# Kernel tuning notes

Hardware: AMD Instinct MI355X
Metric: run time of the kernel (lower is better)

The kernel has to match this reference:

```python
import jax, jax.numpy as jnp
import numpy as np

N, M, A, F = 8000, 12, 64, 64
EPS = 1e-5


def setup_inputs() -> dict:
    key = jax.random.key(0)
    ks = jax.random.split(key, 8)
    rn = lambda k, s, sc=0.05: jax.random.normal(k, s, jnp.float32) * sc
    return {
        "atom_in_fea": rn(ks[0], (N, A), 1.0),
        "nbr_fea": rn(ks[1], (N, M, F), 1.0),
        "nbr_fea_idx": jax.random.randint(ks[2], (N, M), 0, N),
        # fc_full: in = 2A+F, out = 2A (stored as (in, out))
        "W_full": rn(ks[3], (2 * A + F, 2 * A)), "b_full": jnp.zeros((2 * A,), jnp.float32),
        "bn1_gamma": jnp.ones((2 * A,), jnp.float32), "bn1_beta": jnp.zeros((2 * A,), jnp.float32),
        # fc_edge: in = 2A+F, out = 2F
        "W_edge": rn(ks[4], (2 * A + F, 2 * F)), "b_edge": jnp.zeros((2 * F,), jnp.float32),
        "bne_gamma": jnp.ones((2 * F,), jnp.float32), "bne_beta": jnp.zeros((2 * F,), jnp.float32),
        # fc_3body: in = 3A+2F, out = 2A
        "W_3body": rn(ks[5], (3 * A + 2 * F, 2 * A)), "b_3body": jnp.zeros((2 * A,), jnp.float32),
        "bn3_gamma": jnp.ones((2 * A,), jnp.float32), "bn3_beta": jnp.zeros((2 * A,), jnp.float32),
        # bn2 over atom_fea_len
        "bn2_gamma": jnp.ones((A,), jnp.float32), "bn2_beta": jnp.zeros((A,), jnp.float32),
    }


def _bn(x, gamma, beta):
    # training-mode BatchNorm1d: batch stats over all but the last (channel) axis, biased var
    axes = tuple(range(x.ndim - 1))
    mean = jnp.mean(x, axes, keepdims=True)
    var = jnp.mean(jnp.square(x - mean), axes, keepdims=True)
    return (x - mean) * jax.lax.rsqrt(var + EPS) * gamma + beta


def _gate(z, axis):
    filt, core = jnp.split(z, 2, axis=-1)
    return jnp.sum(jax.nn.sigmoid(filt) * jax.nn.softplus(core), axis=axis)


def reference(atom_in_fea, nbr_fea, nbr_fea_idx,
              W_full, b_full, bn1_gamma, bn1_beta,
              W_edge, b_edge, bne_gamma, bne_beta,
              W_3body, b_3body, bn3_gamma, bn3_beta,
              bn2_gamma, bn2_beta):
    a_len = atom_in_fea.shape[1]
    f_len = nbr_fea.shape[2]
    atom_nbr = atom_in_fea[nbr_fea_idx]                       # (N, M, A) gather
    total = jnp.concatenate([
        jnp.broadcast_to(atom_in_fea[:, None, :], atom_nbr.shape),
        atom_nbr, nbr_fea], axis=-1)                           # (N, M, 2A+F)

    # 2-body gated update
    g = _bn(total @ W_full + b_full, bn1_gamma, bn1_beta)      # (N, M, 2A)
    two_body = _gate(g, axis=1)                                # (N, A)

    # explicit edge update
    e = _bn(total @ W_edge + b_edge, bne_gamma, bne_beta)      # (N, M, 2F)
    ef, ec = jnp.split(e, 2, axis=-1)
    nbr_out_fea = nbr_fea + jax.nn.sigmoid(ef) * jax.nn.softplus(ec)

    # 3-body term: Linear over concat([x_i, x_j, x_l, e_ij, e_il]) decomposed so we never
    # materialize the (N, M, M, 3A+2F) concat; only the (N, M, M, 2A) projection exists.
    Wa, Wj, Wl, Wij, Wil = jnp.split(
        W_3body, [a_len, 2 * a_len, 3 * a_len, 3 * a_len + f_len], axis=0)
    p_i = atom_in_fea @ Wa                                     # (N, 2A)
    p_j = atom_nbr @ Wj + nbr_fea @ Wij                        # (N, M, 2A) j/ij part
    p_l = atom_nbr @ Wl + nbr_fea @ Wil                        # (N, M, 2A) l/il part
    z = p_i[:, None, None, :] + p_j[:, :, None, :] + p_l[:, None, :, :] + b_3body
    z = _bn(z, bn3_gamma, bn3_beta)                            # (N, M, M, 2A)
    three_body = _gate(z, axis=(1, 2))                         # (N, A)

    total_summed = _bn(two_body + three_body, bn2_gamma, bn2_beta)
    atom_out_fea = jax.nn.softplus(atom_in_fea + total_summed)
    return (atom_out_fea, nbr_out_fea)
```

## Files before the change

kernel.cpp:

```cpp
#include <hip/hip_runtime.h>

typedef unsigned short u16;
typedef unsigned int u32;
typedef __attribute__((ext_vector_type(8))) short short8;
typedef __attribute__((ext_vector_type(4))) float f32x4;

#define NATOMS 8000
#define MNBR 12
#define EPSV 1e-5f
#define AB 4
#define ROWS 48
#define NBLK 2000
#define K2REC 1664

#define STG_B 12672
__device__ __forceinline__ int stg_idx(int row, int col) {
  return (row >> 2) * 528 + (row & 3) * 128 + col;
}

#define XB_OFF 0
#define WTA_OFF 1024000
#define WTE_OFF 1122304
#define WAT_OFF 1187840
#define SSUM_OFF 1220608
#define PARAMS_OFF 1227776
#define TBUF_OFF 1230848
#define WS_NEED 3278848

#define SS_BN1S 0
#define SS_BN1S2 128
#define SS_BNES 256
#define SS_BNES2 384
#define SS_U2 512
#define SS_V2 640
#define SS_A 768
#define SS_A2 896
#define SS_UB 1024
#define SS_VB 1152
#define SS_AU 1280
#define SS_AV 1408
#define SS_UV 1536

__device__ __forceinline__ u16 f2bf(float f) {
  u32 u = __float_as_uint(f);
  u += 0x7FFFu + ((u >> 16) & 1u);
  return (u16)(u >> 16);
}
__device__ __forceinline__ float bf2f(u16 h) { return __uint_as_float(((u32)h) << 16); }

__device__ __forceinline__ float sigf(float x) {
  return __builtin_amdgcn_rcpf(1.f + __expf(-x));
}
__device__ __forceinline__ float spf(float x) {
  return fmaxf(x, 0.f) + __logf(1.f + __expf(-fabsf(x)));
}

__device__ __forceinline__ void mfma16(f32x4 &acc, short8 a, short8 b) {
  asm volatile("v_mfma_f32_16x16x32_bf16 %0, %1, %2, %0" : "+v"(acc) : "v"(a), "v"(b));
}
__device__ __forceinline__ void accfence(f32x4 &a) {
  asm volatile("s_nop 7\ns_nop 7\ns_nop 7" : "+v"(a));
}
__device__ __forceinline__ void initfence(f32x4 &a) {
  asm volatile("s_nop 1" : "+v"(a));
}

__device__ __forceinline__ void stage_row16(short* lds, int row, int c16, const float* __restrict__ src) {
  const float4* s4 = reinterpret_cast<const float4*>(src);
  float4 q0 = s4[0], q1 = s4[1], q2 = s4[2], q3 = s4[3];
  short8 lo, hi;
  lo[0]=(short)f2bf(q0.x); lo[1]=(short)f2bf(q0.y); lo[2]=(short)f2bf(q0.z); lo[3]=(short)f2bf(q0.w);
  lo[4]=(short)f2bf(q1.x); lo[5]=(short)f2bf(q1.y); lo[6]=(short)f2bf(q1.z); lo[7]=(short)f2bf(q1.w);
  hi[0]=(short)f2bf(q2.x); hi[1]=(short)f2bf(q2.y); hi[2]=(short)f2bf(q2.z); hi[3]=(short)f2bf(q2.w);
  hi[4]=(short)f2bf(q3.x); hi[5]=(short)f2bf(q3.y); hi[6]=(short)f2bf(q3.z); hi[7]=(short)f2bf(q3.w);
  int base = row * 128 + c16 * 2;
  int sw = (row & 7) << 4;
  *reinterpret_cast<short8*>(reinterpret_cast<char*>(lds) + (base ^ sw)) = lo;
  *reinterpret_cast<short8*>(reinterpret_cast<char*>(lds) + ((base + 16) ^ sw)) = hi;
}

__device__ __forceinline__ void stage_xj(const u16* __restrict__ XB, const int* __restrict__ nidx,
                                         int eb, int ab, char* xjT, int t) {
  for (int s = t; s < 512; s += 256) {
    int r = s >> 3, j = s & 7;
    uint4 val = make_uint4(0u, 0u, 0u, 0u);
    if (r < 48) {
      int idx = nidx[eb + r];
      val = *reinterpret_cast<const uint4*>(XB + (size_t)idx * 64 + j * 8);
    } else if (r < 52) {
      val = *reinterpret_cast<const uint4*>(XB + (size_t)(ab + r - 48) * 64 + j * 8);
    }
    int off = (r * 128 + j * 16) ^ ((r & 7) << 4);
    *reinterpret_cast<uint4*>(xjT + off) = val;
  }
}

__device__ __forceinline__ short8 lds_afrag(const char* lds, int row, int kbyte) {
  int off = (row * 128 + kbyte) ^ ((row & 7) << 4);
  return *reinterpret_cast<const short8*>(lds + off);
}

template <int RT>
__device__ __forceinline__ void mfma_dual(const char* xjT, const char* nbrT,
                                          const u16* __restrict__ WTA, const u16* __restrict__ WTE,
                                          int baseA, int baseE, int w, int l,
                                          f32x4 (&acc)[RT][2]) {
  short8 ba[2][2], be[2][2];
#pragma unroll
  for (int p = 0; p < 2; ++p) {
    int colg = ((w + p * 4) << 4) + (l & 15);
#pragma unroll
    for (int kc = 0; kc < 2; ++kc) {
      ba[p][kc] = *reinterpret_cast<const short8*>(WTA + (size_t)(baseA + colg) * 64 + kc * 32 + ((l >> 4) << 3));
      be[p][kc] = *reinterpret_cast<const short8*>(WTE + (size_t)(baseE + colg) * 64 + kc * 32 + ((l >> 4) << 3));
    }
  }
#pragma unroll
  for (int rt = 0; rt < RT; ++rt)
#pragma unroll
    for (int p = 0; p < 2; ++p) { acc[rt][p] = f32x4{0.f, 0.f, 0.f, 0.f}; initfence(acc[rt][p]); }
#pragma unroll
  for (int rt = 0; rt < RT; ++rt) {
    int arow = rt * 16 + (l & 15);
    short8 x0 = lds_afrag(xjT, arow, (l >> 4) << 4);
    short8 x1 = lds_afrag(xjT, arow, 64 + ((l >> 4) << 4));
    short8 n0 = lds_afrag(nbrT, arow, (l >> 4) << 4);
    short8 n1 = lds_afrag(nbrT, arow, 64 + ((l >> 4) << 4));
#pragma unroll
    for (int p = 0; p < 2; ++p) {
      mfma16(acc[rt][p], x0, ba[p][0]);
      mfma16(acc[rt][p], x1, ba[p][1]);
      mfma16(acc[rt][p], n0, be[p][0]);
      mfma16(acc[rt][p], n1, be[p][1]);
    }
  }
#pragma unroll
  for (int rt = 0; rt < RT; ++rt)
#pragma unroll
    for (int p = 0; p < 2; ++p) accfence(acc[rt][p]);
}

__device__ __forceinline__ void mfma_own(const char* xjT, const u16* __restrict__ WTA,
                                         int baseO, int w, int l, float* ownv) {
  short8 bo[2][2];
#pragma unroll
  for (int p = 0; p < 2; ++p) {
    int colg = ((w + p * 4) << 4) + (l & 15);
#pragma unroll
    for (int kc = 0; kc < 2; ++kc)
      bo[p][kc] = *reinterpret_cast<const short8*>(WTA + (size_t)(baseO + colg) * 64 + kc * 32 + ((l >> 4) << 3));
  }
  int arow = 48 + (l & 15);
  short8 x0 = lds_afrag(xjT, arow, (l >> 4) << 4);
  short8 x1 = lds_afrag(xjT, arow, 64 + ((l >> 4) << 4));
  f32x4 acc[2];
#pragma unroll
  for (int p = 0; p < 2; ++p) {
    acc[p] = f32x4{0.f, 0.f, 0.f, 0.f};
    initfence(acc[p]);
    mfma16(acc[p], x0, bo[p][0]);
    mfma16(acc[p], x1, bo[p][1]);
  }
#pragma unroll
  for (int p = 0; p < 2; ++p) accfence(acc[p]);
  if (l < 16) {
    int col0 = (w << 4) + l;
#pragma unroll
    for (int r = 0; r < 4; ++r) {
      ownv[r * 128 + col0] = acc[0][r];
      ownv[r * 128 + col0 + 64] = acc[1][r];
    }
  }
}

__device__ __forceinline__ void aterm_dot(const float* __restrict__ WaT, const float* xown,
                                          int c, int h, float& dv0, float& dv1) {
  const float4* wa4 = reinterpret_cast<const float4*>(WaT + (size_t)c * 64);
  const float4* x0 = reinterpret_cast<const float4*>(xown + (2 * h) * 64);
  const float4* x1 = reinterpret_cast<const float4*>(xown + (2 * h + 1) * 64);
  dv0 = 0.f; dv1 = 0.f;
#pragma unroll
  for (int q = 0; q < 16; ++q) {
    float4 wv = wa4[q], a4 = x0[q], b4 = x1[q];
    dv0 += a4.x * wv.x + a4.y * wv.y + a4.z * wv.z + a4.w * wv.w;
    dv1 += b4.x * wv.x + b4.y * wv.y + b4.z * wv.z + b4.w * wv.w;
  }
}

__global__ __launch_bounds__(256) void k0_prep(const float* __restrict__ atom_in,
                                               const float* __restrict__ W_full,
                                               const float* __restrict__ W_edge,
                                               const float* __restrict__ W_3body,
                                               u16* __restrict__ XB,
                                               u16* __restrict__ WTA, u16* __restrict__ WTE,
                                               float* __restrict__ WaT,
                                               float* __restrict__ ssum) {
  int t = blockIdx.x * 256 + threadIdx.x;
  if (t < 1792) ssum[t] = 0.f;
  if (t < 8192) { int c = t >> 6, k = t & 63; WaT[t] = W_3body[k * 128 + c]; }
  if (t < 49152) {
    int col = t >> 6, k = t & 63;
    int blk = col >> 7, c = col & 127;
    float v;
    switch (blk) {
      case 0: v = W_full[k * 128 + c]; break;
      case 1: v = W_full[(64 + k) * 128 + c]; break;
      case 2: v = W_edge[k * 128 + c]; break;
      case 3: v = W_edge[(64 + k) * 128 + c]; break;
      case 4: v = W_3body[(64 + k) * 128 + c]; break;
      default: v = W_3body[(128 + k) * 128 + c]; break;
    }
    WTA[t] = f2bf(v);
  } else if (t < 81920) {
    int u = t - 49152;
    int col = u >> 6, k = u & 63;
    int blk = col >> 7, c = col & 127;
    float v;
    switch (blk) {
      case 0: v = W_full[(128 + k) * 128 + c]; break;
      case 1: v = W_edge[(128 + k) * 128 + c]; break;
      case 2: v = W_3body[(192 + k) * 128 + c]; break;
      default: v = W_3body[(256 + k) * 128 + c]; break;
    }
    WTE[u] = f2bf(v);
  }
  if (t < NATOMS * 64) XB[t] = f2bf(atom_in[t]);
}

__global__ __launch_bounds__(256, 4) void k2_stats(const float* __restrict__ atom_in,
                                                   const float* __restrict__ nbr_fea,
                                                   const int* __restrict__ nidx,
                                                   const float* __restrict__ WaT,
                                                   const float* __restrict__ b_full,
                                                   const float* __restrict__ b_edge,
                                                   const float* __restrict__ b_3body,
                                                   const u16* __restrict__ XB,
                                                   const u16* __restrict__ WTA,
                                                   const u16* __restrict__ WTE,
                                                   float* __restrict__ k2scr) {
  __shared__ __align__(16) char smem[25088];
  char* nbrT    = smem;
  char* xjT     = smem + 6144;
  float* ownv   = (float*)(smem + 14336);
  float* ubar   = (float*)(smem + 16384);
  float* vbar   = (float*)(smem + 18432);
  float* xown   = (float*)(smem + 20480);
  float* redscr = (float*)(smem + 21504);
  int t = threadIdx.x, l = t & 63, w = t >> 6;
  int ab = blockIdx.x * AB, eb = ab * 12;
  float* sc = k2scr + (size_t)blockIdx.x * K2REC;

  for (int u = t; u < ROWS * 4; u += 256) {
    int row = u >> 2, c16 = (u & 3) * 16;
    stage_row16((short*)nbrT, row, c16, nbr_fea + (size_t)(eb + row) * 64 + c16);
  }
  stage_xj(XB, nidx, eb, ab, xjT, t);
  ubar[t] = 0.f; ubar[256 + t] = 0.f; vbar[t] = 0.f; vbar[256 + t] = 0.f;
  xown[t] = atom_in[(size_t)ab * 64 + t];
  __syncthreads();

  const int baseA[4] = {128, 384, 512, 640};
#pragma unroll
  for (int b = 0; b < 4; ++b) {
    f32x4 acc[3][2];
    mfma_dual<3>(xjT, nbrT, WTA, WTE, baseA[b], b * 128, w, l, acc);
    int col0 = (w << 4) + (l & 15), col1 = col0 + 64;
    int g = l >> 4;
    if (b < 2) {
      mfma_own(xjT, WTA, b ? 256 : 0, w, l, ownv);
      const float* bp = b ? b_edge : b_full;
      float bias0 = bp[col0], bias1 = bp[col1];
      float vs0 = 0.f, vs1 = 0.f, q0 = 0.f, q1 = 0.f;
#pragma unroll
      for (int rt = 0; rt < 3; ++rt) {
        int a12 = (rt * 16 + g * 4) / 12;
        float o0 = ownv[a12 * 128 + col0] + bias0;
        float o1 = ownv[a12 * 128 + col1] + bias1;
#pragma unroll
        for (int r = 0; r < 4; ++r) {
          float v0 = acc[rt][0][r] + o0;
          float v1 = acc[rt][1][r] + o1;
          vs0 += v0; q0 += v0 * v0; vs1 += v1; q1 += v1 * v1;
        }
      }
      vs0 += __shfl_xor(vs0, 16); vs0 += __shfl_xor(vs0, 32);
      vs1 += __shfl_xor(vs1, 16); vs1 += __shfl_xor(vs1, 32);
      q0 += __shfl_xor(q0, 16); q0 += __shfl_xor(q0, 32);
      q1 += __shfl_xor(q1, 16); q1 += __shfl_xor(q1, 32);
      if (l < 16) {
        int base = b ? 256 : 0;
        sc[base + col0] = vs0;
        sc[base + 128 + col0] = q0;
        sc[base + col1] = vs1;
        sc[base + 128 + col1] = q1;
      }
    } else {
      float* uvb = (b == 2) ? ubar : vbar;
      float q0 = 0.f, q1 = 0.f;
#pragma unroll
      for (int rt = 0; rt < 3; ++rt) {
        int a12 = (rt * 16 + g * 4) / 12;
        float s0 = 0.f, s1 = 0.f;
#pragma unroll
        for (int r = 0; r < 4; ++r) {
          float v0 = acc[rt][0][r];
          float v1 = acc[rt][1][r];
          s0 += v0; q0 += v0 * v0; s1 += v1; q1 += v1 * v1;
        }
        atomicAdd(&uvb[a12 * 128 + col0], s0);
        atomicAdd(&uvb[a12 * 128 + col1], s1);
      }
      q0 += __shfl_xor(q0, 16); q0 += __shfl_xor(q0, 32);
      q1 += __shfl_xor(q1, 16); q1 += __shfl_xor(q1, 32);
      if (l < 16) {
        int base = (b == 2) ? SS_U2 : SS_V2;
        sc[base + col0] = q0;
        sc[base + col1] = q1;
      }
    }
  }
  __syncthreads();

  {
    int c = t & 127, h = t >> 7;
    float dv0, dv1;
    aterm_dot(WaT, xown, c, h, dv0, dv1);
    float b3v = b_3body[c];
    float pA = 0.f, pA2 = 0.f, pUb = 0.f, pVb = 0.f, pAU = 0.f, pAV = 0.f, pUV = 0.f;
#pragma unroll
    for (int aa = 0; aa < 2; ++aa) {
      int a = 2 * h + aa;
      float aval = (aa ? dv1 : dv0) + b3v;
      float ub = ubar[a * 128 + c] * (1.f / 12.f);
      float vb = vbar[a * 128 + c] * (1.f / 12.f);
      pA += aval; pA2 += aval * aval; pUb += ub; pVb += vb;
      pAU += aval * ub; pAV += aval * vb; pUV += ub * vb;
    }
    if (h == 1) {
      float* rs = &redscr[c * 7];
      rs[0] = pA; rs[1] = pA2; rs[2] = pUb; rs[3] = pVb; rs[4] = pAU; rs[5] = pAV; rs[6] = pUV;
    }
    __syncthreads();
    if (h == 0) {
      const float* rs = &redscr[c * 7];
      sc[SS_A + c] = pA + rs[0];
      sc[SS_A2 + c] = pA2 + rs[1];
      sc[SS_UB + c] = pUb + rs[2];
      sc[SS_VB + c] = pVb + rs[3];
      sc[SS_AU + c] = pAU + rs[4];
      sc[SS_AV + c] = pAV + rs[5];
      sc[SS_UV + c] = pUV + rs[6];
    }
  }
}

__global__ __launch_bounds__(256) void k3r_reduce(const float* __restrict__ k2scr,
                                                  float* __restrict__ ssum) {
  int cb = blockIdx.x & 1, ch = blockIdx.x >> 1;
  int f = cb * 256 + threadIdx.x;
  if (f >= K2REC / 4) return;
  int r0 = ch * 32;
  if (r0 >= NBLK) return;
  int r1 = min(r0 + 32, NBLK);
  float s0 = 0.f, s1 = 0.f, s2 = 0.f, s3 = 0.f;
#pragma unroll 8
  for (int r = r0; r < r1; ++r) {
    float4 v = *reinterpret_cast<const float4*>(k2scr + (size_t)r * K2REC + f * 4);
    s0 += v.x; s1 += v.y; s2 += v.z; s3 += v.w;
  }
  atomicAdd(&ssum[f * 4 + 0], s0);
  atomicAdd(&ssum[f * 4 + 1], s1);
  atomicAdd(&ssum[f * 4 + 2], s2);
  atomicAdd(&ssum[f * 4 + 3], s3);
}

__global__ void k3p_params(const float* __restrict__ ssum,
                           const float* __restrict__ g1, const float* __restrict__ be1,
                           const float* __restrict__ ge, const float* __restrict__ bee,
                           const float* __restrict__ g3, const float* __restrict__ be3,
                           float* __restrict__ params) {
  int c = threadIdx.x;
  if (c >= 128) return;
  const float cnt1 = 1.f / 96000.f;
  {
    float m = ssum[SS_BN1S + c] * cnt1;
    float var = ssum[SS_BN1S2 + c] * cnt1 - m * m;
    float s = g1[c] * rsqrtf(fmaxf(var, 0.f) + EPSV);
    params[c] = s; params[128 + c] = be1[c] - m * s;
  }
  {
    float m = ssum[SS_BNES + c] * cnt1;
    float var = ssum[SS_BNES2 + c] * cnt1 - m * m;
    float s = ge[c] * rsqrtf(fmaxf(var, 0.f) + EPSV);
    params[256 + c] = s; params[384 + c] = bee[c] - m * s;
  }
  {
    float Nf = (float)NATOMS;
    float A_ = ssum[SS_A + c], A2 = ssum[SS_A2 + c];
    float U2 = ssum[SS_U2 + c], V2 = ssum[SS_V2 + c];
    float Ub = ssum[SS_UB + c], Vb = ssum[SS_VB + c];
    float AU = ssum[SS_AU + c], AV = ssum[SS_AV + c], UV = ssum[SS_UV + c];
    float m = (A_ + Ub + Vb) / Nf;
    float ez2 = A2 / Nf + (U2 + V2) / (Nf * 12.f) + 2.f * (AU + AV + UV) / Nf;
    float var = ez2 - m * m;
    float s = g3[c] * rsqrtf(fmaxf(var, 0.f) + EPSV);
    params[512 + c] = s; params[640 + c] = be3[c] - m * s;
  }
}

__global__ __launch_bounds__(256, 4) void k4_main(const float* __restrict__ atom_in,
                                                  const float* __restrict__ nbr_fea,
                                                  const int* __restrict__ nidx,
                                                  const float* __restrict__ WaT,
                                                  const float* __restrict__ b_full,
                                                  const float* __restrict__ b_edge,
                                                  const float* __restrict__ b_3body,
                                                  const u16* __restrict__ XB,
                                                  const u16* __restrict__ WTA,
                                                  const u16* __restrict__ WTE,
                                                  const float* __restrict__ params,
                                                  float* __restrict__ tbuf,
                                                  float* __restrict__ out_nbr,
                                                  float* __restrict__ bn2scr) {
  __shared__ __align__(16) char smem[36224];
  char* nbrT      = smem;
  char* xjT       = smem + 6144;
  u16* u_s        = (u16*)(smem + 14336);
  float* ownv     = (float*)(smem + 27008);
  float* t2buf    = (float*)(smem + 29056);
  float* params_s = (float*)(smem + 30080);
  float* p3_s     = (float*)(smem + 32128);
  float* a_s      = (float*)(smem + 33152);
  float* xown     = (float*)(smem + 35200);
  u16* v_s        = (u16*)smem;
  float* redscr2  = (float*)(smem + 14336);
  int t = threadIdx.x, l = t & 63, w = t >> 6;
  int ab = blockIdx.x * AB, eb = ab * 12;

  for (int u = t; u < ROWS * 4; u += 256) {
    int row = u >> 2, c16 = (u & 3) * 16;
    stage_row16((short*)nbrT, row, c16, nbr_fea + (size_t)(eb + row) * 64 + c16);
  }
  stage_xj(XB, nidx, eb, ab, xjT, t);
  xown[t] = atom_in[(size_t)ab * 64 + t];
  params_s[t] = params[t];
  params_s[t + 256] = params[t + 256];
  p3_s[t] = params[512 + t];
  t2buf[t] = 0.f;
  __syncthreads();

  {
    int c = t & 127, h = t >> 7;
    float dv0, dv1;
    aterm_dot(WaT, xown, c, h, dv0, dv1);
    float s3 = p3_s[c], t3 = p3_s[128 + c];
    float b3v = b_3body[c];
    a_s[(2 * h) * 128 + c] = (dv0 + b3v) * s3 + t3;
    a_s[(2 * h + 1) * 128 + c] = (dv1 + b3v) * s3 + t3;
  }

#pragma unroll
  for (int b = 0; b < 2; ++b) {
    f32x4 acc[3][2];
    mfma_dual<3>(xjT, nbrT, WTA, WTE, b ? 384 : 128, b * 128, w, l, acc);
    mfma_own(xjT, WTA, b ? 256 : 0, w, l, ownv);
    int col0 = (w << 4) + (l & 15), col1 = col0 + 64;
    int g = l >> 4;
    const float* bp = b ? b_edge : b_full;
    float bias0 = bp[col0], bias1 = bp[col1];
    float sc0 = params_s[b * 256 + col0], sh0 = params_s[b * 256 + 128 + col0];
    float sc1 = params_s[b * 256 + col1], sh1 = params_s[b * 256 + 128 + col1];
#pragma unroll
    for (int rt = 0; rt < 3; ++rt) {
      int a12 = (rt * 16 + g * 4) / 12;
      float o0 = ownv[a12 * 128 + col0] + bias0;
      float o1 = ownv[a12 * 128 + col1] + bias1;
      float gsum = 0.f;
#pragma unroll
      for (int r = 0; r < 4; ++r) {
        int row = rt * 16 + g * 4 + r;
        float v0 = acc[rt][0][r] + o0;
        float v1 = acc[rt][1][r] + o1;
        float gate = sigf(v0 * sc0 + sh0) * spf(v1 * sc1 + sh1);
        if (b == 0) {
          gsum += gate;
        } else {
          size_t eg = (size_t)(eb + row) * 64 + col0;
          out_nbr[eg] = nbr_fea[eg] + gate;
        }
      }
      if (b == 0) atomicAdd(&t2buf[a12 * 64 + col0], gsum);
    }
  }

  {
    f32x4 acc[3][2];
    mfma_dual<3>(xjT, nbrT, WTA, WTE, 512, 256, w, l, acc);
    int col0 = (w << 4) + (l & 15), col1 = col0 + 64;
    int g = l >> 4;
    float s30 = p3_s[col0], s31 = p3_s[col1];
#pragma unroll
    for (int rt = 0; rt < 3; ++rt) {
#pragma unroll
      for (int r = 0; r < 4; ++r) {
        int row = rt * 16 + g * 4 + r;
        u_s[stg_idx(row, col0)] = f2bf(acc[rt][0][r] * s30);
        u_s[stg_idx(row, col1)] = f2bf(acc[rt][1][r] * s31);
      }
    }
  }
  {
    f32x4 acc[3][2];
    mfma_dual<3>(xjT, nbrT, WTA, WTE, 640, 384, w, l, acc);
    __syncthreads();
    int col0 = (w << 4) + (l & 15), col1 = col0 + 64;
    int g = l >> 4;
    float s30 = p3_s[col0], s31 = p3_s[col1];
#pragma unroll
    for (int rt = 0; rt < 3; ++rt) {
#pragma unroll
      for (int r = 0; r < 4; ++r) {
        int row = rt * 16 + g * 4 + r;
        v_s[stg_idx(row, col0)] = f2bf(acc[rt][0][r] * s30);
        v_s[stg_idx(row, col1)] = f2bf(acc[rt][1][r] * s31);
      }
    }
  }
  __syncthreads();

  float acc3 = 0.f;
  {
    int c = l, a = w;
    float af = a_s[a * 128 + c], ac = a_s[a * 128 + 64 + c];
    float Fl[12], Hl[12];
#pragma unroll
    for (int j2 = 0; j2 < 12; ++j2) {
      float vf = bf2f(v_s[stg_idx(a * 12 + j2, c)]);
      float vc = bf2f(v_s[stg_idx(a * 12 + j2, 64 + c)]);
      Fl[j2] = __expf(-vf);
      Hl[j2] = __expf(vc);
    }
    for (int j = 0; j < 12; ++j) {
      float uf = bf2f(u_s[stg_idx(a * 12 + j, c)]);
      float uc = bf2f(u_s[stg_idx(a * 12 + j, 64 + c)]);
      float Ej = __expf(-(af + uf));
      float Gj = __expf(ac + uc);
#pragma unroll
      for (int l2 = 0; l2 < 12; ++l2) {
        float p = fmaf(Ej, Fl[l2], 1.f);
        float q = fmaf(Gj, Hl[l2], 1.f);
        acc3 += __builtin_amdgcn_rcpf(p) * __log2f(q);
      }
    }
  }
  __syncthreads();

  {
    float x = t2buf[t] + acc3 * 0.6931471805599453f;
    tbuf[(size_t)(ab + w) * 64 + l] = x;
    redscr2[t] = x;
    redscr2[256 + t] = x * x;
    __syncthreads();
    if (t < 64) {
      float s = redscr2[t] + redscr2[t + 64] + redscr2[t + 128] + redscr2[t + 192];
      float s2 = redscr2[256 + t] + redscr2[256 + t + 64] + redscr2[256 + t + 128] + redscr2[256 + t + 192];
      bn2scr[(size_t)t * 2048 + blockIdx.x] = s;
      bn2scr[(size_t)(64 + t) * 2048 + blockIdx.x] = s2;
    }
  }
}

__global__ __launch_bounds__(256) void k5_reduce(const float* __restrict__ bn2scr,
                                                 float* __restrict__ bn2sum) {
  __shared__ float wsum[4];
  int c = blockIdx.x, t = threadIdx.x;
  float s = 0.f;
#pragma unroll 4
  for (int i = t; i < NBLK; i += 256) s += bn2scr[(size_t)c * 2048 + i];
  s += __shfl_xor(s, 1); s += __shfl_xor(s, 2); s += __shfl_xor(s, 4);
  s += __shfl_xor(s, 8); s += __shfl_xor(s, 16); s += __shfl_xor(s, 32);
  if ((t & 63) == 0) wsum[t >> 6] = s;
  __syncthreads();
  if (t == 0) bn2sum[c] = wsum[0] + wsum[1] + wsum[2] + wsum[3];
}

__global__ __launch_bounds__(256) void k6_out(const float* __restrict__ atom_in,
                                              const float* __restrict__ tbuf,
                                              const float* __restrict__ bn2sum,
                                              const float* __restrict__ g2,
                                              const float* __restrict__ be2,
                                              float* __restrict__ out_atom) {
  __shared__ float sc[64], sh[64];
  int t = threadIdx.x;
  if (t < 64) {
    float S = bn2sum[t], S2 = bn2sum[64 + t];
    float m = S * (1.f / (float)NATOMS);
    float var = S2 * (1.f / (float)NATOMS) - m * m;
    float s = g2[t] * rsqrtf(fmaxf(var, 0.f) + EPSV);
    sc[t] = s; sh[t] = be2[t] - m * s;
  }
  __syncthreads();
  int i = blockIdx.x * 256 + t;
  if (i < NATOMS * 64) {
    int c = i & 63;
    float v = atom_in[i] + tbuf[i] * sc[c] + sh[c];
    out_atom[i] = spf(v);
  }
}

extern "C" void kernel_launch(void* const* d_in, const int* in_sizes, int n_in,
                              void* d_out, int out_size, void* d_ws, size_t ws_size,
                              hipStream_t stream) {
  if (ws_size < (size_t)WS_NEED) return;
  const float* atom_in = (const float*)d_in[0];
  const float* nbr_fea = (const float*)d_in[1];
  const int* nidx = (const int*)d_in[2];
  const float* W_full = (const float*)d_in[3];
  const float* b_full = (const float*)d_in[4];
  const float* g1 = (const float*)d_in[5];
  const float* be1 = (const float*)d_in[6];
  const float* W_edge = (const float*)d_in[7];
  const float* b_edge = (const float*)d_in[8];
  const float* ge = (const float*)d_in[9];
  const float* bee = (const float*)d_in[10];
  const float* W_3body = (const float*)d_in[11];
  const float* b_3body = (const float*)d_in[12];
  const float* g3 = (const float*)d_in[13];
  const float* be3 = (const float*)d_in[14];
  const float* g2 = (const float*)d_in[15];
  const float* be2 = (const float*)d_in[16];

  char* ws = (char*)d_ws;
  u16* XB = (u16*)(ws + XB_OFF);
  u16* WTA = (u16*)(ws + WTA_OFF);
  u16* WTE = (u16*)(ws + WTE_OFF);
  float* WaT = (float*)(ws + WAT_OFF);
  float* ssum = (float*)(ws + SSUM_OFF);
  float* bn2sum = ssum + K2REC;
  float* params = (float*)(ws + PARAMS_OFF);
  float* tbuf = (float*)(ws + TBUF_OFF);

  float* out_atom = (float*)d_out;
  float* out_nbr = out_atom + NATOMS * 64;
  float* k2scr = out_nbr;
  float* bn2scr = out_atom;

  k0_prep<<<2000, 256, 0, stream>>>(atom_in, W_full, W_edge, W_3body, XB, WTA, WTE, WaT, ssum);
  k2_stats<<<NBLK, 256, 0, stream>>>(atom_in, nbr_fea, nidx, WaT, b_full, b_edge, b_3body,
                                     XB, WTA, WTE, k2scr);
  k3r_reduce<<<128, 256, 0, stream>>>(k2scr, ssum);
  k3p_params<<<1, 128, 0, stream>>>(ssum, g1, be1, ge, bee, g3, be3, params);
  k4_main<<<NBLK, 256, 0, stream>>>(atom_in, nbr_fea, nidx, WaT, b_full, b_edge, b_3body,
                                    XB, WTA, WTE, params, tbuf, out_nbr, bn2scr);
  k5_reduce<<<128, 256, 0, stream>>>(bn2scr, bn2sum);
  k6_out<<<2000, 256, 0, stream>>>(atom_in, tbuf, bn2sum, g2, be2, out_atom);
}
```

Measured before the change: 169.2 us.

## Compute BN statistics via Gram matrix of edge inputs instead of per-edge projections

Replaces the stats pass, which projected every edge through all weight blocks, with one that accumulates a 128x128 Gram matrix of concatenated [x_j, e_ij] inputs plus per-atom sums. Second moments then come from w^T M w in a small new kernel, and first moments and cross terms from projecting per-atom sums. This cuts the stats-pass MFMA work and register pressure, at the cost of global atomics into 8 replicated Gram copies, two extra small kernels, and bf16 rounding of summed inputs. The quadratic-form step also changes numerical behaviour compared with direct accumulation.

Measured after the change: 164.3 us. 1.03x faster.

```diff
diff --git a/kernel.cpp b/kernel.cpp
--- a/kernel.cpp
+++ b/kernel.cpp
@@ -11,7 +11,8 @@
 #define AB 4
 #define ROWS 48
 #define NBLK 2000
-#define K2REC 1664
+#define NZG 500
+#define KREC 1408
 
 #define STG_B 12672
 __device__ __forceinline__ int stg_idx(int row, int col) {
@@ -20,26 +21,27 @@
 
 #define XB_OFF 0
 #define WTA_OFF 1024000
-#define WTE_OFF 1122304
-#define WAT_OFF 1187840
-#define SSUM_OFF 1220608
-#define PARAMS_OFF 1227776
-#define TBUF_OFF 1230848
-#define WS_NEED 3278848
+#define WTE_OFF 1138688
+#define WAT_OFF 1204224
+#define MREP_OFF 1236992
+#define MFIN_OFF 1761280
+#define QF4_OFF 1826816
+#define SSUM_OFF 1828864
+#define PARAMS_OFF 1835008
+#define TBUF_OFF 1838080
+#define WS_NEED 3886080
 
 #define SS_BN1S 0
 #define SS_BN1S2 128
 #define SS_BNES 256
 #define SS_BNES2 384
-#define SS_U2 512
-#define SS_V2 640
-#define SS_A 768
-#define SS_A2 896
-#define SS_UB 1024
-#define SS_VB 1152
-#define SS_AU 1280
-#define SS_AV 1408
-#define SS_UV 1536
+#define SS_A 512
+#define SS_A2 640
+#define SS_UB 768
+#define SS_VB 896
+#define SS_AU 1024
+#define SS_AV 1152
+#define SS_UV 1280
 
 __device__ __forceinline__ u16 f2bf(float f) {
   u32 u = __float_as_uint(f);
@@ -100,6 +102,15 @@
   return *reinterpret_cast<const short8*>(lds + off);
 }
 
+__device__ __forceinline__ void zt_w16(char* zT, int chan, int e, u16 v) {
+  int off = (chan * 128 + e * 2) ^ ((chan & 7) << 4);
+  *reinterpret_cast<u16*>(zT + off) = v;
+}
+__device__ __forceinline__ u16 zt_r16(const char* zT, int chan, int e) {
+  int off = (chan * 128 + e * 2) ^ ((chan & 7) << 4);
+  return *reinterpret_cast<const u16*>(zT + off);
+}
+
 template <int RT>
 __device__ __forceinline__ void mfma_dual(const char* xjT, const char* nbrT,
                                           const u16* __restrict__ WTA, const u16* __restrict__ WTE,
@@ -132,6 +143,38 @@
       mfma16(acc[rt][p], x1, ba[p][1]);
       mfma16(acc[rt][p], n0, be[p][0]);
       mfma16(acc[rt][p], n1, be[p][1]);
+    }
+  }
+#pragma unroll
+  for (int rt = 0; rt < RT; ++rt)
+#pragma unroll
+    for (int p = 0; p < 2; ++p) accfence(acc[rt][p]);
+}
+
+template <int RT>
+__device__ __forceinline__ void mfma_single(const char* aT, const u16* __restrict__ WTA,
+                                            int baseC, int w, int l, f32x4 (&acc)[RT][2]) {
+  short8 bw[2][2];
+#pragma unroll
+  for (int p = 0; p < 2; ++p) {
+    int colg = ((w + p * 4) << 4) + (l & 15);
+#pragma unroll
+    for (int kc = 0; kc < 2; ++kc)
+      bw[p][kc] = *reinterpret_cast<const short8*>(WTA + (size_t)(baseC + colg) * 64 + kc * 32 + ((l >> 4) << 3));
+  }
+#pragma unroll
+  for (int rt = 0; rt < RT; ++rt)
+#pragma unroll
+    for (int p = 0; p < 2; ++p) { acc[rt][p] = f32x4{0.f, 0.f, 0.f, 0.f}; initfence(acc[rt][p]); }
+#pragma unroll
+  for (int rt = 0; rt < RT; ++rt) {
+    int arow = rt * 16 + (l & 15);
+    short8 x0 = lds_afrag(aT, arow, (l >> 4) << 4);
+    short8 x1 = lds_afrag(aT, arow, 64 + ((l >> 4) << 4));
+#pragma unroll
+    for (int p = 0; p < 2; ++p) {
+      mfma16(acc[rt][p], x0, bw[p][0]);
+      mfma16(acc[rt][p], x1, bw[p][1]);
     }
   }
 #pragma unroll
@@ -194,11 +237,13 @@
                                                u16* __restrict__ XB,
                                                u16* __restrict__ WTA, u16* __restrict__ WTE,
                                                float* __restrict__ WaT,
+                                               float* __restrict__ Mrep,
                                                float* __restrict__ ssum) {
   int t = blockIdx.x * 256 + threadIdx.x;
-  if (t < 1792) ssum[t] = 0.f;
+  if (t < 1536) ssum[t] = 0.f;
+  if (t < 131072) Mrep[t] = 0.f;
   if (t < 8192) { int c = t >> 6, k = t & 63; WaT[t] = W_3body[k * 128 + c]; }
-  if (t < 49152) {
+  if (t < 57344) {
     int col = t >> 6, k = t & 63;
     int blk = col >> 7, c = col & 127;
     float v;
@@ -208,11 +253,12 @@
       case 2: v = W_edge[k * 128 + c]; break;
       case 3: v = W_edge[(64 + k) * 128 + c]; break;
       case 4: v = W_3body[(64 + k) * 128 + c]; break;
-      default: v = W_3body[(128 + k) * 128 + c]; break;
+      case 5: v = W_3body[(128 + k) * 128 + c]; break;
+      default: v = W_3body[k * 128 + c]; break;
     }
     WTA[t] = f2bf(v);
-  } else if (t < 81920) {
-    int u = t - 49152;
+  } else if (t < 57344 + 32768) {
+    int u = t - 57344;
     int col = u >> 6, k = u & 63;
     int blk = col >> 7, c = col & 127;
     float v;
@@ -227,154 +273,236 @@
   if (t < NATOMS * 64) XB[t] = f2bf(atom_in[t]);
 }
 
-__global__ __launch_bounds__(256, 4) void k2_stats(const float* __restrict__ atom_in,
-                                                   const float* __restrict__ nbr_fea,
-                                                   const int* __restrict__ nidx,
-                                                   const float* __restrict__ WaT,
-                                                   const float* __restrict__ b_full,
-                                                   const float* __restrict__ b_edge,
-                                                   const float* __restrict__ b_3body,
-                                                   const u16* __restrict__ XB,
-                                                   const u16* __restrict__ WTA,
-                                                   const u16* __restrict__ WTE,
-                                                   float* __restrict__ k2scr) {
-  __shared__ __align__(16) char smem[25088];
-  char* nbrT    = smem;
-  char* xjT     = smem + 6144;
-  float* ownv   = (float*)(smem + 14336);
-  float* ubar   = (float*)(smem + 16384);
-  float* vbar   = (float*)(smem + 18432);
-  float* xown   = (float*)(smem + 20480);
-  float* redscr = (float*)(smem + 21504);
+__global__ __launch_bounds__(256, 4) void kzg_stats(const float* __restrict__ nbr_fea,
+                                                    const int* __restrict__ nidx,
+                                                    const float* __restrict__ b_full,
+                                                    const float* __restrict__ b_edge,
+                                                    const float* __restrict__ b_3body,
+                                                    const u16* __restrict__ XB,
+                                                    const u16* __restrict__ WTA,
+                                                    const u16* __restrict__ WTE,
+                                                    float* __restrict__ Mrep,
+                                                    float* __restrict__ krec) {
+  __shared__ __align__(16) char smem[30720];
+  char* zT       = smem;
+  char* xT       = smem + 16384;
+  char* ZxT      = smem + 18432;
+  char* ZnT      = smem + 20480;
+  float* Zbar    = (float*)(smem + 22528);
   int t = threadIdx.x, l = t & 63, w = t >> 6;
-  int ab = blockIdx.x * AB, eb = ab * 12;
-  float* sc = k2scr + (size_t)blockIdx.x * K2REC;
-
-  for (int u = t; u < ROWS * 4; u += 256) {
-    int row = u >> 2, c16 = (u & 3) * 16;
-    stage_row16((short*)nbrT, row, c16, nbr_fea + (size_t)(eb + row) * 64 + c16);
-  }
-  stage_xj(XB, nidx, eb, ab, xjT, t);
-  ubar[t] = 0.f; ubar[256 + t] = 0.f; vbar[t] = 0.f; vbar[256 + t] = 0.f;
-  xown[t] = atom_in[(size_t)ab * 64 + t];
+  int bid = blockIdx.x;
+  int ab = bid * 16;
+  float* sc = krec + (size_t)bid * KREC;
+
+  if (t < 128) {
+    int row = t >> 3, j = t & 7;
+    uint4 val = *reinterpret_cast<const uint4*>(XB + (size_t)(ab + row) * 64 + j * 8);
+    int off = (row * 128 + j * 16) ^ ((row & 7) << 4);
+    *reinterpret_cast<uint4*>(xT + off) = val;
+  }
+  for (int s = t; s < 2048; s += 256) Zbar[s] = 0.f;
+  for (int s = t; s < 512; s += 256) {
+    int chan = s >> 2, kq = 48 + (s & 3) * 4;
+    int off = (chan * 128 + kq * 2) ^ ((chan & 7) << 4);
+    *reinterpret_cast<uint2*>(zT + off) = make_uint2(0u, 0u);
+  }
+
+  f32x4 gacc[2][8];
+#pragma unroll
+  for (int h = 0; h < 2; ++h)
+#pragma unroll
+    for (int q = 0; q < 8; ++q) { gacc[h][q] = f32x4{0.f, 0.f, 0.f, 0.f}; initfence(gacc[h][q]); }
+
+  for (int c4 = 0; c4 < 4; ++c4) {
+    __syncthreads();
+    int ebg = (ab + c4 * 4) * 12;
+    for (int s = t; s < 384; s += 256) {
+      int r = s >> 3, j = s & 7;
+      int idx = nidx[ebg + r];
+      uint4 val = *reinterpret_cast<const uint4*>(XB + (size_t)idx * 64 + j * 8);
+      const u16* v8 = reinterpret_cast<const u16*>(&val);
+#pragma unroll
+      for (int q2 = 0; q2 < 8; ++q2) zt_w16(zT, j * 8 + q2, r, v8[q2]);
+    }
+    for (int s = t; s < 768; s += 256) {
+      int e = s >> 4, cq = (s & 15) * 4;
+      float4 v = *reinterpret_cast<const float4*>(nbr_fea + (size_t)(ebg + e) * 64 + cq);
+      zt_w16(zT, 64 + cq + 0, e, f2bf(v.x));
+      zt_w16(zT, 64 + cq + 1, e, f2bf(v.y));
+      zt_w16(zT, 64 + cq + 2, e, f2bf(v.z));
+      zt_w16(zT, 64 + cq + 3, e, f2bf(v.w));
+    }
+    __syncthreads();
+#pragma unroll
+    for (int h = 0; h < 2; ++h) {
+      int ta = w + h * 4;
+      short8 a0 = lds_afrag(zT, ta * 16 + (l & 15), (l >> 4) << 4);
+      short8 a1 = lds_afrag(zT, ta * 16 + (l & 15), 64 + ((l >> 4) << 4));
+#pragma unroll
+      for (int q = 0; q < 8; ++q) {
+        short8 b0 = lds_afrag(zT, q * 16 + (l & 15), (l >> 4) << 4);
+        short8 b1 = lds_afrag(zT, q * 16 + (l & 15), 64 + ((l >> 4) << 4));
+        mfma16(gacc[h][q], a0, b0);
+        mfma16(gacc[h][q], a1, b1);
+      }
+    }
+    for (int s = t; s < 512; s += 256) {
+      int a4 = s >> 7, c = s & 127;
+      float acc = 0.f;
+#pragma unroll
+      for (int m = 0; m < 12; ++m) acc += bf2f(zt_r16(zT, c, a4 * 12 + m));
+      Zbar[(c4 * 4 + a4) * 128 + c] += acc;
+    }
+  }
+#pragma unroll
+  for (int h = 0; h < 2; ++h)
+#pragma unroll
+    for (int q = 0; q < 8; ++q) accfence(gacc[h][q]);
+
+  float* Md = Mrep + (size_t)(bid & 7) * 16384;
+#pragma unroll
+  for (int h = 0; h < 2; ++h) {
+    int ta = w + h * 4;
+#pragma unroll
+    for (int q = 0; q < 8; ++q)
+#pragma unroll
+      for (int r = 0; r < 4; ++r) {
+        int Mrow = ta * 16 + (l >> 4) * 4 + r;
+        int Mcol = q * 16 + (l & 15);
+        atomicAdd(&Md[Mrow * 128 + Mcol], gacc[h][q][r]);
+      }
+  }
+
   __syncthreads();
-
-  const int baseA[4] = {128, 384, 512, 640};
-#pragma unroll
-  for (int b = 0; b < 4; ++b) {
-    f32x4 acc[3][2];
-    mfma_dual<3>(xjT, nbrT, WTA, WTE, baseA[b], b * 128, w, l, acc);
-    int col0 = (w << 4) + (l & 15), col1 = col0 + 64;
-    int g = l >> 4;
-    if (b < 2) {
-      mfma_own(xjT, WTA, b ? 256 : 0, w, l, ownv);
-      const float* bp = b ? b_edge : b_full;
-      float bias0 = bp[col0], bias1 = bp[col1];
-      float vs0 = 0.f, vs1 = 0.f, q0 = 0.f, q1 = 0.f;
-#pragma unroll
-      for (int rt = 0; rt < 3; ++rt) {
-        int a12 = (rt * 16 + g * 4) / 12;
-        float o0 = ownv[a12 * 128 + col0] + bias0;
-        float o1 = ownv[a12 * 128 + col1] + bias1;
-#pragma unroll
-        for (int r = 0; r < 4; ++r) {
-          float v0 = acc[rt][0][r] + o0;
-          float v1 = acc[rt][1][r] + o1;
-          vs0 += v0; q0 += v0 * v0; vs1 += v1; q1 += v1 * v1;
-        }
-      }
-      vs0 += __shfl_xor(vs0, 16); vs0 += __shfl_xor(vs0, 32);
-      vs1 += __shfl_xor(vs1, 16); vs1 += __shfl_xor(vs1, 32);
-      q0 += __shfl_xor(q0, 16); q0 += __shfl_xor(q0, 32);
-      q1 += __shfl_xor(q1, 16); q1 += __shfl_xor(q1, 32);
-      if (l < 16) {
-        int base = b ? 256 : 0;
-        sc[base + col0] = vs0;
-        sc[base + 128 + col0] = q0;
-        sc[base + col1] = vs1;
-        sc[base + 128 + col1] = q1;
-      }
-    } else {
-      float* uvb = (b == 2) ? ubar : vbar;
-      float q0 = 0.f, q1 = 0.f;
-#pragma unroll
-      for (int rt = 0; rt < 3; ++rt) {
-        int a12 = (rt * 16 + g * 4) / 12;
-        float s0 = 0.f, s1 = 0.f;
-#pragma unroll
-        for (int r = 0; r < 4; ++r) {
-          float v0 = acc[rt][0][r];
-          float v1 = acc[rt][1][r];
-          s0 += v0; q0 += v0 * v0; s1 += v1; q1 += v1 * v1;
-        }
-        atomicAdd(&uvb[a12 * 128 + col0], s0);
-        atomicAdd(&uvb[a12 * 128 + col1], s1);
-      }
-      q0 += __shfl_xor(q0, 16); q0 += __shfl_xor(q0, 32);
-      q1 += __shfl_xor(q1, 16); q1 += __shfl_xor(q1, 32);
-      if (l < 16) {
-        int base = (b == 2) ? SS_U2 : SS_V2;
-        sc[base + col0] = q0;
-        sc[base + col1] = q1;
-      }
-    }
+  {
+    int row = t >> 4, kq = (t & 15) * 4;
+    const float* zr = &Zbar[row * 128 + kq];
+    u16 vx[4], vn[4];
+#pragma unroll
+    for (int i = 0; i < 4; ++i) { vx[i] = f2bf(zr[i]); vn[i] = f2bf(zr[64 + i]); }
+    int off = (row * 128 + kq * 2) ^ ((row & 7) << 4);
+    *reinterpret_cast<uint2*>(ZxT + off) = *reinterpret_cast<uint2*>(vx);
+    *reinterpret_cast<uint2*>(ZnT + off) = *reinterpret_cast<uint2*>(vn);
   }
   __syncthreads();
 
-  {
-    int c = t & 127, h = t >> 7;
-    float dv0, dv1;
-    aterm_dot(WaT, xown, c, h, dv0, dv1);
-    float b3v = b_3body[c];
-    float pA = 0.f, pA2 = 0.f, pUb = 0.f, pVb = 0.f, pAU = 0.f, pAV = 0.f, pUV = 0.f;
-#pragma unroll
-    for (int aa = 0; aa < 2; ++aa) {
-      int a = 2 * h + aa;
-      float aval = (aa ? dv1 : dv0) + b3v;
-      float ub = ubar[a * 128 + c] * (1.f / 12.f);
-      float vb = vbar[a * 128 + c] * (1.f / 12.f);
-      pA += aval; pA2 += aval * aval; pUb += ub; pVb += vb;
-      pAU += aval * ub; pAV += aval * vb; pUV += ub * vb;
-    }
-    if (h == 1) {
-      float* rs = &redscr[c * 7];
-      rs[0] = pA; rs[1] = pA2; rs[2] = pUb; rs[3] = pVb; rs[4] = pAU; rs[5] = pAV; rs[6] = pUV;
-    }
+  f32x4 qf[1][2], qe[1][2], qu[1][2], qv[1][2], o1[1][2], oe[1][2], a3[1][2];
+  mfma_dual<1>(ZxT, ZnT, WTA, WTE, 128, 0, w, l, qf);
+  mfma_dual<1>(ZxT, ZnT, WTA, WTE, 384, 128, w, l, qe);
+  mfma_dual<1>(ZxT, ZnT, WTA, WTE, 512, 256, w, l, qu);
+  mfma_dual<1>(ZxT, ZnT, WTA, WTE, 640, 384, w, l, qv);
+  mfma_single<1>(xT, WTA, 0, w, l, o1);
+  mfma_single<1>(xT, WTA, 256, w, l, oe);
+  mfma_single<1>(xT, WTA, 768, w, l, a3);
+
+#pragma unroll
+  for (int p = 0; p < 2; ++p) {
+    int col = (w << 4) + (l & 15) + p * 64;
+    float bf = b_full[col], be_ = b_edge[col], b3 = b_3body[col];
+    float s1 = 0.f, s1q = 0.f, se = 0.f, seq = 0.f;
+    float A = 0.f, A2 = 0.f, UB = 0.f, VB = 0.f, AU = 0.f, AV = 0.f, UV = 0.f;
+#pragma unroll
+    for (int r = 0; r < 4; ++r) {
+      float o = o1[0][p][r] + bf;
+      float q = qf[0][p][r];
+      s1 += 12.f * o + q; s1q += 12.f * o * o + 2.f * o * q;
+      float oev = oe[0][p][r] + be_;
+      float qev = qe[0][p][r];
+      se += 12.f * oev + qev; seq += 12.f * oev * oev + 2.f * oev * qev;
+      float av = a3[0][p][r] + b3;
+      float ub = qu[0][p][r] * (1.f / 12.f);
+      float vb = qv[0][p][r] * (1.f / 12.f);
+      A += av; A2 += av * av; UB += ub; VB += vb;
+      AU += av * ub; AV += av * vb; UV += ub * vb;
+    }
+    float st[11] = {s1, s1q, se, seq, A, A2, UB, VB, AU, AV, UV};
+#pragma unroll
+    for (int i = 0; i < 11; ++i) {
+      st[i] += __shfl_xor(st[i], 16);
+      st[i] += __shfl_xor(st[i], 32);
+    }
+    if (l < 16) {
+      sc[SS_BN1S + col] = st[0];
+      sc[SS_BN1S2 + col] = st[1];
+      sc[SS_BNES + col] = st[2];
+      sc[SS_BNES2 + col] = st[3];
+      sc[SS_A + col] = st[4];
+      sc[SS_A2 + col] = st[5];
+      sc[SS_UB + col] = st[6];
+      sc[SS_VB + col] = st[7];
+      sc[SS_AU + col] = st[8];
+      sc[SS_AV + col] = st[9];
+      sc[SS_UV + col] = st[10];
+    }
+  }
+}
+
+__global__ __launch_bounds__(256) void k3r_reduce(const float* __restrict__ krec,
+                                                  const float* __restrict__ Mrep,
+                                                  float* __restrict__ ssum,
+                                                  float* __restrict__ Mfin) {
+  int bid = blockIdx.x, t = threadIdx.x;
+  if (bid < 20) {
+    int cb = bid & 1, chunk = bid >> 1;
+    int f = cb * 256 + t;
+    if (f >= KREC / 4) return;
+    int r0 = chunk * 50, r1 = r0 + 50;
+    float s0 = 0.f, s1 = 0.f, s2 = 0.f, s3 = 0.f;
+#pragma unroll 5
+    for (int r = r0; r < r1; ++r) {
+      float4 v = *reinterpret_cast<const float4*>(krec + (size_t)r * KREC + f * 4);
+      s0 += v.x; s1 += v.y; s2 += v.z; s3 += v.w;
+    }
+    atomicAdd(&ssum[f * 4 + 0], s0);
+    atomicAdd(&ssum[f * 4 + 1], s1);
+    atomicAdd(&ssum[f * 4 + 2], s2);
+    atomicAdd(&ssum[f * 4 + 3], s3);
+  } else {
+    int idx = (bid - 20) * 256 + t;
+    if (idx >= 16384) return;
+    float s = 0.f;
+#pragma unroll
+    for (int rep = 0; rep < 8; ++rep) s += Mrep[(size_t)rep * 16384 + idx];
+    Mfin[idx] = s;
+  }
+}
+
+__global__ __launch_bounds__(128) void k3q_qf(const float* __restrict__ M,
+                                              const float* __restrict__ W_full,
+                                              const float* __restrict__ W_edge,
+                                              const float* __restrict__ W_3body,
+                                              float* __restrict__ qf4) {
+  __shared__ float wv[128];
+  __shared__ float red[2];
+  int c = blockIdx.x, t = threadIdx.x;
+#pragma unroll
+  for (int sel = 0; sel < 4; ++sel) {
+    float wval;
+    if (sel == 0) wval = (t < 64) ? W_full[(64 + t) * 128 + c] : W_full[(64 + t) * 128 + c];
+    else if (sel == 1) wval = W_edge[(64 + t) * 128 + c];
+    else if (sel == 2) wval = (t < 64) ? W_3body[(64 + t) * 128 + c] : W_3body[(128 + t) * 128 + c];
+    else wval = (t < 64) ? W_3body[(128 + t) * 128 + c] : W_3body[(192 + t) * 128 + c];
+    wv[t] = wval;
     __syncthreads();
-    if (h == 0) {
-      const float* rs = &redscr[c * 7];
-      sc[SS_A + c] = pA + rs[0];
-      sc[SS_A2 + c] = pA2 + rs[1];
-      sc[SS_UB + c] = pUb + rs[2];
-      sc[SS_VB + c] = pVb + rs[3];
-      sc[SS_AU + c] = pAU + rs[4];
-      sc[SS_AV + c] = pAV + rs[5];
-      sc[SS_UV + c] = pUV + rs[6];
-    }
-  }
-}
-
-__global__ __launch_bounds__(256) void k3r_reduce(const float* __restrict__ k2scr,
-                                                  float* __restrict__ ssum) {
-  int cb = blockIdx.x & 1, ch = blockIdx.x >> 1;
-  int f = cb * 256 + threadIdx.x;
-  if (f >= K2REC / 4) return;
-  int r0 = ch * 32;
-  if (r0 >= NBLK) return;
-  int r1 = min(r0 + 32, NBLK);
-  float s0 = 0.f, s1 = 0.f, s2 = 0.f, s3 = 0.f;
+    float y = 0.f;
+    const float4* mr = reinterpret_cast<const float4*>(M + (size_t)t * 128);
 #pragma unroll 8
-  for (int r = r0; r < r1; ++r) {
-    float4 v = *reinterpret_cast<const float4*>(k2scr + (size_t)r * K2REC + f * 4);
-    s0 += v.x; s1 += v.y; s2 += v.z; s3 += v.w;
-  }
-  atomicAdd(&ssum[f * 4 + 0], s0);
-  atomicAdd(&ssum[f * 4 + 1], s1);
-  atomicAdd(&ssum[f * 4 + 2], s2);
-  atomicAdd(&ssum[f * 4 + 3], s3);
+    for (int q2 = 0; q2 < 32; ++q2) {
+      float4 mv = mr[q2];
+      y += mv.x * wv[q2 * 4] + mv.y * wv[q2 * 4 + 1] + mv.z * wv[q2 * 4 + 2] + mv.w * wv[q2 * 4 + 3];
+    }
+    float pr = y * wv[t];
+    pr += __shfl_xor(pr, 1); pr += __shfl_xor(pr, 2); pr += __shfl_xor(pr, 4);
+    pr += __shfl_xor(pr, 8); pr += __shfl_xor(pr, 16); pr += __shfl_xor(pr, 32);
+    if ((t & 63) == 0) red[t >> 6] = pr;
+    __syncthreads();
+    if (t == 0) qf4[sel * 128 + c] = red[0] + red[1];
+    __syncthreads();
+  }
 }
 
 __global__ void k3p_params(const float* __restrict__ ssum,
+                           const float* __restrict__ qf4,
                            const float* __restrict__ g1, const float* __restrict__ be1,
                            const float* __restrict__ ge, const float* __restrict__ bee,
                            const float* __restrict__ g3, const float* __restrict__ be3,
@@ -384,20 +512,20 @@
   const float cnt1 = 1.f / 96000.f;
   {
     float m = ssum[SS_BN1S + c] * cnt1;
-    float var = ssum[SS_BN1S2 + c] * cnt1 - m * m;
+    float var = (ssum[SS_BN1S2 + c] + qf4[c]) * cnt1 - m * m;
     float s = g1[c] * rsqrtf(fmaxf(var, 0.f) + EPSV);
     params[c] = s; params[128 + c] = be1[c] - m * s;
   }
   {
     float m = ssum[SS_BNES + c] * cnt1;
-    float var = ssum[SS_BNES2 + c] * cnt1 - m * m;
+    float var = (ssum[SS_BNES2 + c] + qf4[128 + c]) * cnt1 - m * m;
     float s = ge[c] * rsqrtf(fmaxf(var, 0.f) + EPSV);
     params[256 + c] = s; params[384 + c] = bee[c] - m * s;
   }
   {
     float Nf = (float)NATOMS;
     float A_ = ssum[SS_A + c], A2 = ssum[SS_A2 + c];
-    float U2 = ssum[SS_U2 + c], V2 = ssum[SS_V2 + c];
+    float U2 = qf4[256 + c], V2 = qf4[384 + c];
     float Ub = ssum[SS_UB + c], Vb = ssum[SS_VB + c];
     float AU = ssum[SS_AU + c], AV = ssum[SS_AV + c], UV = ssum[SS_UV + c];
     float m = (A_ + Ub + Vb) / Nf;
@@ -635,21 +763,26 @@
   u16* WTA = (u16*)(ws + WTA_OFF);
   u16* WTE = (u16*)(ws + WTE_OFF);
   float* WaT = (float*)(ws + WAT_OFF);
+  float* Mrep = (float*)(ws + MREP_OFF);
+  float* Mfin = (float*)(ws + MFIN_OFF);
+  float* qf4 = (float*)(ws + QF4_OFF);
   float* ssum = (float*)(ws + SSUM_OFF);
-  float* bn2sum = ssum + K2REC;
+  float* bn2sum = ssum + KREC;
   float* params = (float*)(ws + PARAMS_OFF);
   float* tbuf = (float*)(ws + TBUF_OFF);
 
   float* out_atom = (float*)d_out;
   float* out_nbr = out_atom + NATOMS * 64;
-  float* k2scr = out_nbr;
+  float* krec = out_nbr;
   float* bn2scr = out_atom;
 
-  k0_prep<<<2000, 256, 0, stream>>>(atom_in, W_full, W_edge, W_3body, XB, WTA, WTE, WaT, ssum);
-  k2_stats<<<NBLK, 256, 0, stream>>>(atom_in, nbr_fea, nidx, WaT, b_full, b_edge, b_3body,
-                                     XB, WTA, WTE, k2scr);
-  k3r_reduce<<<128, 256, 0, stream>>>(k2scr, ssum);
-  k3p_params<<<1, 128, 0, stream>>>(ssum, g1, be1, ge, bee, g3, be3, params);
+  k0_prep<<<2000, 256, 0, stream>>>(atom_in, W_full, W_edge, W_3body, XB, WTA, WTE, WaT,
+                                    Mrep, ssum);
+  kzg_stats<<<NZG, 256, 0, stream>>>(nbr_fea, nidx, b_full, b_edge, b_3body,
+                                     XB, WTA, WTE, Mrep, krec);
+  k3r_reduce<<<84, 256, 0, stream>>>(krec, Mrep, ssum, Mfin);
+  k3q_qf<<<128, 128, 0, stream>>>(Mfin, W_full, W_edge, W_3body, qf4);
+  k3p_params<<<1, 128, 0, stream>>>(ssum, qf4, g1, be1, ge, bee, g3, be3, params);
   k4_main<<<NBLK, 256, 0, stream>>>(atom_in, nbr_fea, nidx, WaT, b_full, b_edge, b_3body,
                                     XB, WTA, WTE, params, tbuf, out_nbr, bn2scr);
   k5_reduce<<<128, 256, 0, stream>>>(bn2scr, bn2sum);
```
